# Optimization experiments

Hardware: AMD Instinct MI355X
Metric: run time of the kernel (lower is better)

The kernel has to match this reference:

```python
import jax, jax.numpy as jnp
import numpy as np

B, D_IN, D_HID, D_OUT = 16384, 512, 512, 512
E, K = 8, 2
VQ_COEFF, LB_COEFF = 0.05, 0.01
LOG100 = float(np.log(100.0))
LOG2 = float(np.log(2.0))


def _normalize(v):
    # torch F.normalize(dim=1): x / max(||x||, 1e-12)
    n = jnp.linalg.norm(v, axis=-1, keepdims=True)
    return v / jnp.maximum(n, 1e-12)


def _cv_squared(v):
    # torch .var() is unbiased (ddof=1)
    return jnp.var(v, ddof=1) / (jnp.mean(v) ** 2 + 1e-10)


def _rbm_layer(x, rm, W, b, ca, temp):
    # x: [B, d_in], rm: [E, d_in], W: [E, d_out, d_in], b: [E, d_out]
    rm_n = jax.lax.stop_gradient(_normalize(rm))          # .detach() in source
    nx = _normalize(x)
    dists = nx @ rm_n.T                                    # [B, E]
    top_v, top_i = jax.lax.top_k(dists, K)                 # [B, K]
    tv = jax.nn.softmax(top_v, axis=-1)                    # softmax over top-k
    bsz = dists.shape[0]
    attn = jnp.zeros_like(dists).at[jnp.arange(bsz)[:, None], top_i].set(tv)
    # const_attention is frozen (requires_grad=False)
    inp_att = jnp.exp(jnp.minimum(jax.lax.stop_gradient(ca), LOG100))  # [E]
    # dense gather-compute-scatter: expert e output for every token, masked by attn
    eo = jnp.einsum('bi,eoi->beo', x, W) * inp_att[None, :, None] + b[None, :, :]
    out = jnp.einsum('be,beo->bo', jax.lax.stop_gradient(attn), eo)    # att.detach()
    out = out * jnp.exp(jnp.minimum(temp, LOG100))
    # aux losses (eval mode: no EMA memory update)
    vq = -(nx[:, None, :] * rm_n[top_i]).sum(-1)           # [B, K]
    vq_loss = (tv * vq).sum(-1).mean()
    lb = _cv_squared(attn.sum(0))
    aux = VQ_COEFF * vq_loss + LB_COEFF * lb               # sim_coeff = 0
    return out, aux


def setup_inputs() -> dict:
    key = jax.random.key(0)
    ks = jax.random.split(key, 8)
    x = jax.random.normal(ks[0], (B, D_IN), dtype=jnp.float32)
    rm0 = _normalize(jax.random.normal(ks[1], (E, D_IN), dtype=jnp.float32))
    W0 = jax.random.normal(ks[2], (E, D_HID, D_IN), dtype=jnp.float32) / np.sqrt(D_IN)
    b0 = jnp.zeros((E, D_HID), dtype=jnp.float32)
    rm1 = _normalize(jax.random.normal(ks[3], (E, D_HID), dtype=jnp.float32))
    W1 = jax.random.normal(ks[4], (E, D_OUT, D_HID), dtype=jnp.float32) / np.sqrt(D_HID)
    b1 = jnp.zeros((E, D_OUT), dtype=jnp.float32)
    temp0 = jnp.full((1,), LOG2, dtype=jnp.float32)
    temp1 = jnp.full((1,), LOG2, dtype=jnp.float32)
    ca0 = jnp.zeros((E,), dtype=jnp.float32)
    ca1 = jnp.zeros((E,), dtype=jnp.float32)
    return {"x": x, "rm0": rm0, "W0": W0, "b0": b0, "temp0": temp0, "ca0": ca0,
            "rm1": rm1, "W1": W1, "b1": b1, "temp1": temp1, "ca1": ca1}


def reference(x, rm0, W0, b0, temp0, ca0, rm1, W1, b1, temp1, ca1):
    h0, a0 = _rbm_layer(x, rm0, W0, b0, ca0, temp0)
    h_emb = h0                      # embedding tapped after layer 0 (pre-activation)
    h = jax.nn.relu(h0)             # norm_type=None -> no norm
    h1, a1 = _rbm_layer(h, rm1, W1, b1, ca1, temp1)
    return (h_emb, h1, a0 + a1)
```

## Files before the change

kernel.cpp:

```cpp
#include <hip/hip_runtime.h>
#include <cmath>
#include <cstdint>

#define NTOK   16384
#define NEXP   8
#define DM     512
#define LOG100 4.605170185988092f

typedef _Float16 half8  __attribute__((ext_vector_type(8)));
typedef float    floatx4 __attribute__((ext_vector_type(4)));

#define MFMA_F16(a, b, c) __builtin_amdgcn_mfma_f32_16x16x32_f16((a), (b), (c), 0, 0, 0)

__device__ __forceinline__ void gl_lds16(const void* g, void* l) {
    __builtin_amdgcn_global_load_lds(
        (const __attribute__((address_space(1))) void*)g,
        (__attribute__((address_space(3))) void*)l, 16, 0, 0);
}

__device__ __forceinline__ void atomAddF(float* p, float v) {
#if __has_builtin(__builtin_amdgcn_global_atomic_fadd_f32)
    __builtin_amdgcn_global_atomic_fadd_f32((__attribute__((address_space(1))) float*)p, v);
#else
    atomicAdd(p, v);
#endif
}


__global__ __launch_bounds__(256) void pack_w_kernel(
    const float* __restrict__ W0, const float* __restrict__ W1,
    half8* __restrict__ w0pk, half8* __restrict__ w1pk,
    const float* __restrict__ rm0, const float* __restrict__ rm1,
    const float* __restrict__ ca0, const float* __restrict__ ca1,
    const float* __restrict__ temp0, const float* __restrict__ temp1,
    float* __restrict__ ctrl, float* __restrict__ rmn)
{
    if (blockIdx.x == 3072) {
        int tid = threadIdx.x, lane = tid & 63, w = tid >> 6;
        if (tid < 32) ((int*)ctrl)[tid] = 0;
        if (tid >= 32 && tid < 48) ctrl[tid] = 0.f;
        if (tid == 48 || tid == 49) ctrl[tid] = 0.f;
        if (tid == 50) ctrl[50] = expf(fminf(temp0[0], LOG100));
        if (tid == 51) ctrl[51] = expf(fminf(temp1[0], LOG100));
        if (tid >= 52 && tid < 68) {
            int i = tid - 52;
            ctrl[tid] = expf(fminf(i < 8 ? ca0[i] : ca1[i - 8], LOG100));
        }
        for (int r = w; r < 16; r += 4) {
            const float* src = (r < 8) ? (rm0 + r * DM) : (rm1 + (r - 8) * DM);
            float v[8]; float ss = 0.f;
            #pragma unroll
            for (int j = 0; j < 8; ++j) { v[j] = src[lane + 64 * j]; ss += v[j] * v[j]; }
            #pragma unroll
            for (int off = 32; off > 0; off >>= 1) ss += __shfl_xor(ss, off);
            float inv = 1.f / fmaxf(sqrtf(ss), 1e-12f);
            float* dst = rmn + r * DM;
            #pragma unroll
            for (int j = 0; j < 8; ++j) dst[lane + 64 * j] = v[j] * inv;
        }
        return;
    }
    int i = blockIdx.x * 256 + threadIdx.x;
    if (i < 512 * 1024) {
        int l = i & 63, j = (i >> 6) & 15, kb = (i >> 10) & 15, nt = (i >> 14) & 3, e = i >> 16;
        int s = l >> 3, p = l & 7, c = p ^ s;
        int n = nt * 128 + j * 8 + s;
        int k = kb * 32 + (c & 3) * 8;
        const float* src = W0 + ((size_t)e * DM + n) * DM + k;
        half8 v;
        #pragma unroll
        for (int t = 0; t < 8; ++t) {
            float f = src[t];
            _Float16 h = (_Float16)f;
            v[t] = (c < 4) ? h : (_Float16)(f - (float)h);
        }
        w0pk[i] = v;
    } else {
        int m = i - 512 * 1024;
        int l = m & 63, j = (m >> 6) & 15, kb = (m >> 10) & 7, nt = (m >> 13) & 3, e = m >> 15;
        int s = l >> 3, p = l & 7, c = p ^ s;
        int n = nt * 128 + j * 8 + s;
        int k = kb * 64 + c * 8;
        const float* src = W1 + ((size_t)e * DM + n) * DM + k;
        half8 v;
        #pragma unroll
        for (int t = 0; t < 8; ++t) v[t] = (_Float16)src[t];
        w1pk[m] = v;
    }
}

__global__ __launch_bounds__(256) void route_kernel(
    const float* __restrict__ src,
    const float* __restrict__ rmn,
    int relu_in, int split,
    _Float16* __restrict__ dst,
    unsigned char* __restrict__ key,
    float2* __restrict__ wts,
    float2* __restrict__ bs,
    float* __restrict__ zrow)
{
    __shared__ float rmLds[NEXP * DM];
    int tid = threadIdx.x;
    for (int i = tid; i < NEXP * DM; i += 256) rmLds[i] = rmn[i];
    __syncthreads();
    int lane = tid & 63, w = tid >> 6;
    int token = blockIdx.x * 4 + w;

    {
        float4 z4 = {0.f, 0.f, 0.f, 0.f};
        float4* zp = (float4*)(zrow + (size_t)token * DM);
        zp[lane] = z4;
        zp[lane + 64] = z4;
    }

    const float* row = src + (size_t)token * DM;
    float x[8]; float ss = 0.f;
    #pragma unroll
    for (int j = 0; j < 8; ++j) {
        float v = row[lane + 64 * j];
        if (relu_in) v = fmaxf(v, 0.f);
        x[j] = v; ss += v * v;
    }
    if (split) {
        #pragma unroll
        for (int j = 0; j < 8; ++j) {
            int k = lane + 64 * j;
            size_t base = (size_t)token * 1024 + (size_t)((k >> 5) << 6) + (k & 31);
            _Float16 h = (_Float16)x[j];
            dst[base] = h;
            dst[base + 32] = (_Float16)(x[j] - (float)h);
        }
    } else {
        #pragma unroll
        for (int j = 0; j < 8; ++j)
            dst[(size_t)token * DM + lane + 64 * j] = (_Float16)x[j];
    }
    float d[8];
    #pragma unroll
    for (int e = 0; e < 8; ++e) {
        float a = 0.f;
        #pragma unroll
        for (int j = 0; j < 8; ++j) a += x[j] * rmLds[e * DM + lane + 64 * j];
        d[e] = a;
    }
    #pragma unroll
    for (int off = 32; off > 0; off >>= 1) {
        ss += __shfl_xor(ss, off);
        #pragma unroll
        for (int e = 0; e < 8; ++e) d[e] += __shfl_xor(d[e], off);
    }
    float inv = 1.f / fmaxf(sqrtf(ss), 1e-12f);
    float best = -1e30f, second = -1e30f; int be = 0, se = 0;
    #pragma unroll
    for (int e = 0; e < 8; ++e) {
        float de = d[e] * inv;
        if (de > best)        { second = best; se = be; best = de; be = e; }
        else if (de > second) { second = de; se = e; }
    }
    float z = expf(second - best);
    float w0 = 1.f / (1.f + z), w1 = z / (1.f + z);
    if (lane == 0) {
        key[token] = (unsigned char)be;
        key[NTOK + token] = (unsigned char)se;
        wts[token] = make_float2(w0, w1);
        bs[token] = make_float2(best, second);
    }
}

__global__ __launch_bounds__(256) void compact_kernel(
    const unsigned char* __restrict__ key,
    const float2* __restrict__ wts,
    const float2* __restrict__ bs,
    int* __restrict__ cnt,
    unsigned short* __restrict__ bkt,
    float* __restrict__ imp,
    float* __restrict__ vq_acc)
{
    int slot = blockIdx.x >> 3, e = blockIdx.x & 7;
    int chunk = blockIdx.y;
    const unsigned char* k = key + slot * NTOK;
    unsigned short* ob = bkt + (size_t)(slot * 8 + e) * NTOK;
    int tid = threadIdx.x, lane = tid & 63, w = tid >> 6;
    float wsum = 0.f, vqs = 0.f;
    for (int c = 0; c < 8; ++c) {
        int tok = chunk * 2048 + c * 256 + tid;
        bool m = (k[tok] == (unsigned char)e);
        unsigned long long mask = __ballot(m);
        int wcount = __popcll(mask);
        int wbase = 0;
        if (lane == 0 && wcount) wbase = atomicAdd(&cnt[slot * 8 + e], wcount);
        wbase = __shfl(wbase, 0);
        if (m) {
            int pre = __popcll(mask & ((1ull << lane) - 1ull));
            ob[wbase + pre] = (unsigned short)tok;
            float2 wp = wts[tok]; float2 b2 = bs[tok];
            float wv = slot ? wp.y : wp.x;
            wsum += wv;
            vqs  += wv * (slot ? b2.y : b2.x);
        }
    }
    #pragma unroll
    for (int off = 32; off > 0; off >>= 1) {
        wsum += __shfl_xor(wsum, off);
        vqs  += __shfl_xor(vqs, off);
    }
    __shared__ float rw[4], rv[4];
    if (lane == 0) { rw[w] = wsum; rv[w] = vqs; }
    __syncthreads();
    if (tid == 0) {
        atomicAdd(&imp[e], rw[0] + rw[1] + rw[2] + rw[3]);
        atomicAdd(vq_acc, -(rv[0] + rv[1] + rv[2] + rv[3]));
    }
}

template <bool SPLIT>
__global__ __launch_bounds__(256, 4) void gemm_kernel(
    const _Float16* __restrict__ A,
    const _Float16* __restrict__ Wpk,
    const float* __restrict__ bias,
    const float* __restrict__ iav,
    const float* __restrict__ tscp,
    const int* __restrict__ cnt16,
    const unsigned short* __restrict__ bkt,
    const float2* __restrict__ wts,
    float* __restrict__ outp)
{
    __shared__ __align__(16) _Float16 ldsB[2 * 8192];
    __shared__ int tokLds[128];

    int p = blockIdx.x;
    int xcd = p & 7, s = p >> 3;
    int t = xcd * 34 + (s >> 2), nt = s & 3;
    int b = -1, m0 = 0, M = 0, acc0 = 0;
    #pragma unroll
    for (int bb = 0; bb < 16; ++bb) {
        int Me = cnt16[bb];
        int ne = (Me + 127) >> 7;
        if (t >= acc0 && t < acc0 + ne) { b = bb; m0 = (t - acc0) << 7; M = Me; }
        acc0 += ne;
    }
    if (b < 0) return;
    int slot = b >> 3, e = b & 7;
    int n0 = nt << 7;
    int valid = min(128, M - m0);
    int tid = threadIdx.x, lane = tid & 63, w = tid >> 6;
    if (tid < 128) tokLds[tid] = bkt[(size_t)b * NTOK + m0 + min(tid, valid - 1)];
    __syncthreads();

    int wm = w >> 1, wn = w & 1;
    int r0 = wm * 64, c0 = wn * 64;
    int q = lane >> 4, l15 = lane & 15;

    constexpr int KIT = SPLIT ? 16 : 8;
    constexpr int AS  = SPLIT ? 1024 : 512;

    const _Float16* Ab[4];
    #pragma unroll
    for (int mi = 0; mi < 4; ++mi)
        Ab[mi] = A + (size_t)tokLds[r0 + mi * 16 + l15] * AS + q * 8;

    const _Float16* wtile = Wpk + (size_t)(e * 4 + nt) * KIT * 8192;

    floatx4 accu[4][4];
    #pragma unroll
    for (int mi = 0; mi < 4; ++mi)
        #pragma unroll
        for (int ni = 0; ni < 4; ++ni) accu[mi][ni] = (floatx4){0.f, 0.f, 0.f, 0.f};

    #pragma unroll
    for (int jj = 0; jj < 4; ++jj) {
        int j = w + jj * 4;
        gl_lds16(wtile + j * 512 + lane * 8, (void*)(ldsB + j * 512));
    }

    #pragma unroll
    for (int kb = 0; kb < KIT; ++kb) {
        half8 ah[4], al[4];
        #pragma unroll
        for (int mi = 0; mi < 4; ++mi) {
            ah[mi] = *(const half8*)(Ab[mi] + kb * 64);
            al[mi] = *(const half8*)(Ab[mi] + kb * 64 + 32);
        }
        if (kb + 1 < KIT) {
            _Float16* dB = ldsB + ((kb + 1) & 1) * 8192;
            const _Float16* wb = wtile + (size_t)(kb + 1) * 8192;
            #pragma unroll
            for (int jj = 0; jj < 4; ++jj) {
                int j = w + jj * 4;
                gl_lds16(wb + j * 512 + lane * 8, (void*)(dB + j * 512));
            }
        }
        if (kb + 1 < KIT) asm volatile("s_waitcnt vmcnt(12)" ::: "memory");
        else              asm volatile("s_waitcnt vmcnt(8)"  ::: "memory");
        __builtin_amdgcn_sched_barrier(0);
        __builtin_amdgcn_s_barrier();
        {
            const _Float16* bB = ldsB + (kb & 1) * 8192;
            #pragma unroll
            for (int ni = 0; ni < 4; ++ni) {
                int r = c0 + ni * 16 + l15;
                int ph = q ^ (r & 7), pl = (q + 4) ^ (r & 7);
                half8 bh = *(const half8*)(bB + r * 64 + ph * 8);
                half8 bl = *(const half8*)(bB + r * 64 + pl * 8);
                if constexpr (SPLIT) {
                    #pragma unroll
                    for (int mi = 0; mi < 4; ++mi) accu[mi][ni] = MFMA_F16(ah[mi], bh, accu[mi][ni]);
                    #pragma unroll
                    for (int mi = 0; mi < 4; ++mi) accu[mi][ni] = MFMA_F16(ah[mi], bl, accu[mi][ni]);
                    #pragma unroll
                    for (int mi = 0; mi < 4; ++mi) accu[mi][ni] = MFMA_F16(al[mi], bh, accu[mi][ni]);
                } else {
                    #pragma unroll
                    for (int mi = 0; mi < 4; ++mi) accu[mi][ni] = MFMA_F16(ah[mi], bh, accu[mi][ni]);
                    #pragma unroll
                    for (int mi = 0; mi < 4; ++mi) accu[mi][ni] = MFMA_F16(al[mi], bl, accu[mi][ni]);
                }
            }
        }
        if (kb + 1 < KIT) {
            __builtin_amdgcn_sched_barrier(0);
            __builtin_amdgcn_s_barrier();
        }
    }

    float tsc = *tscp, iae = iav[e];
    float bv[4];
    #pragma unroll
    for (int ni = 0; ni < 4; ++ni) bv[ni] = bias[e * DM + n0 + c0 + ni * 16 + l15];
    #pragma unroll
    for (int mi = 0; mi < 4; ++mi) {
        int liBase = r0 + mi * 16 + q * 4;
        #pragma unroll
        for (int reg = 0; reg < 4; ++reg) {
            int li = liBase + reg;
            if (li < valid) {
                int tok = tokLds[li];
                float2 wp = wts[tok];
                float wgt = slot ? wp.y : wp.x;
                float sg = tsc * wgt * iae, sb = tsc * wgt;
                float* orow = outp + (size_t)tok * DM + n0;
                #pragma unroll
                for (int ni = 0; ni < 4; ++ni) {
                    float v = accu[mi][ni][reg] * sg + bv[ni] * sb;
                    int c = c0 + ni * 16 + l15;
                    atomAddF(&orow[c], v);
                }
            }
        }
    }
}

__global__ void finalize_kernel(const float* __restrict__ ctrl, float* __restrict__ outp)
{
    if (threadIdx.x == 0) {
        float aux = 0.f;
        for (int l = 0; l < 2; ++l) {
            float vq = ctrl[48 + l] / (float)NTOK;
            float mean = 0.f;
            for (int e = 0; e < 8; ++e) mean += ctrl[32 + l * 8 + e];
            mean *= 0.125f;
            float s = 0.f;
            for (int e = 0; e < 8; ++e) {
                float d = ctrl[32 + l * 8 + e] - mean;
                s += d * d;
            }
            float var = s / 7.f;
            float lb = var / (mean * mean + 1e-10f);
            aux += 0.05f * vq + 0.01f * lb;
        }
        *outp = aux;
    }
}

extern "C" void kernel_launch(void* const* d_in, const int* in_sizes, int n_in,
                              void* d_out, int out_size, void* d_ws, size_t ws_size,
                              hipStream_t stream) {
    const float* x     = (const float*)d_in[0];
    const float* rm0   = (const float*)d_in[1];
    const float* W0    = (const float*)d_in[2];
    const float* b0    = (const float*)d_in[3];
    const float* temp0 = (const float*)d_in[4];
    const float* ca0   = (const float*)d_in[5];
    const float* rm1   = (const float*)d_in[6];
    const float* W1    = (const float*)d_in[7];
    const float* b1    = (const float*)d_in[8];
    const float* temp1 = (const float*)d_in[9];
    const float* ca1   = (const float*)d_in[10];
    float* out = (float*)d_out;

    char* ws = (char*)d_ws;
    float* ctrl = (float*)ws;
    int*   cnt  = (int*)ctrl;
    float* imp  = ctrl + 32;
    float* vq   = ctrl + 48;
    float* tsc  = ctrl + 50;
    float* ia   = ctrl + 52;
    float* rmn  = ctrl + 128;
    float2*        wts = (float2*)(ws + (size_t)64  * 1024);
    float2*        bs  = (float2*)(ws + (size_t)384 * 1024);
    unsigned char* key = (unsigned char*)(ws + (size_t)704 * 1024);

    char* big = ws + (1 << 20);
    half8*          w0pk8 = (half8*)(big);
    half8*          w1pk8 = (half8*)(big + (size_t)8  * 1024 * 1024);
    const _Float16* w0pk  = (const _Float16*)w0pk8;
    const _Float16* w1pk  = (const _Float16*)w1pk8;
    _Float16*       h16   = (_Float16*)(big + (size_t)12 * 1024 * 1024);
    unsigned short* bkt   = (unsigned short*)(big + (size_t)28 * 1024 * 1024);

    _Float16* xpk = (_Float16*)(out + (size_t)NTOK * DM);

    pack_w_kernel<<<3073, 256, 0, stream>>>(W0, W1, w0pk8, w1pk8,
        rm0, rm1, ca0, ca1, temp0, temp1, ctrl, rmn);

    route_kernel<<<4096, 256, 0, stream>>>(x, rmn, 0, 1, xpk, key, wts, bs, out);
    compact_kernel<<<dim3(16, 8), 256, 0, stream>>>(key, wts, bs, cnt, bkt, imp, vq);
    gemm_kernel<true><<<1088, 256, 0, stream>>>(xpk, w0pk, b0, ia, tsc,
        cnt, bkt, wts, out);

    route_kernel<<<4096, 256, 0, stream>>>(out, rmn + 4096, 1, 0, h16,
        key + 2 * NTOK, wts + NTOK, bs + NTOK, out + (size_t)NTOK * DM);
    compact_kernel<<<dim3(16, 8), 256, 0, stream>>>(key + 2 * NTOK, wts + NTOK, bs + NTOK,
        cnt + 16, bkt + 16 * NTOK, imp + 8, vq + 1);
    gemm_kernel<false><<<1088, 256, 0, stream>>>(h16, w1pk, b1, ia + 8, tsc + 1,
        cnt + 16, bkt + 16 * NTOK, wts + NTOK, out + (size_t)NTOK * DM);

    finalize_kernel<<<1, 64, 0, stream>>>(ctrl, out + (size_t)2 * NTOK * DM);
}
```

Measured before the change: 460.6 us.

## Switch grouped GEMM to single-wave 64x64 tiles with register-prefetched A

The grouped expert GEMM changes from 256-thread blocks computing 128x128 tiles to single-wavefront blocks computing 64x64 tiles. The grid grows to 528*8 blocks and the XCD-aware block remapping is removed. Because one wave owns its LDS buffers, the per-k-step barriers go away. A-fragments are now double-buffered in registers so the next k-step's gathered A loads overlap the MFMAs. Each block reuses less of B and A, so global and L2 traffic rises and there are more redundant loads, in exchange for better load balance across uneven expert buckets and no barrier stalls.

```diff
diff --git a/kernel.cpp b/kernel.cpp
--- a/kernel.cpp
+++ b/kernel.cpp
@@ -214,7 +214,7 @@
 }
 
 template <bool SPLIT>
-__global__ __launch_bounds__(256, 4) void gemm_kernel(
+__global__ __launch_bounds__(64) void gemm_kernel(
     const _Float16* __restrict__ A,
     const _Float16* __restrict__ Wpk,
     const float* __restrict__ bias,
@@ -225,31 +225,27 @@
     const float2* __restrict__ wts,
     float* __restrict__ outp)
 {
-    __shared__ __align__(16) _Float16 ldsB[2 * 8192];
-    __shared__ int tokLds[128];
-
-    int p = blockIdx.x;
-    int xcd = p & 7, s = p >> 3;
-    int t = xcd * 34 + (s >> 2), nt = s & 3;
+    __shared__ __align__(16) _Float16 ldsB[2 * 4096];
+    __shared__ int tokLds[64];
+
+    int bx = blockIdx.x;
+    int t = bx >> 3, nt64 = bx & 7;
     int b = -1, m0 = 0, M = 0, acc0 = 0;
     #pragma unroll
     for (int bb = 0; bb < 16; ++bb) {
         int Me = cnt16[bb];
-        int ne = (Me + 127) >> 7;
-        if (t >= acc0 && t < acc0 + ne) { b = bb; m0 = (t - acc0) << 7; M = Me; }
+        int ne = (Me + 63) >> 6;
+        if (t >= acc0 && t < acc0 + ne) { b = bb; m0 = (t - acc0) << 6; M = Me; }
         acc0 += ne;
     }
     if (b < 0) return;
     int slot = b >> 3, e = b & 7;
-    int n0 = nt << 7;
-    int valid = min(128, M - m0);
-    int tid = threadIdx.x, lane = tid & 63, w = tid >> 6;
-    if (tid < 128) tokLds[tid] = bkt[(size_t)b * NTOK + m0 + min(tid, valid - 1)];
-    __syncthreads();
-
-    int wm = w >> 1, wn = w & 1;
-    int r0 = wm * 64, c0 = wn * 64;
+    int n0 = nt64 << 6;
+    int valid = min(64, M - m0);
+    int lane = threadIdx.x;
     int q = lane >> 4, l15 = lane & 15;
+
+    tokLds[lane] = bkt[(size_t)b * NTOK + m0 + min(lane, valid - 1)];
 
     constexpr int KIT = SPLIT ? 16 : 8;
     constexpr int AS  = SPLIT ? 1024 : 512;
@@ -257,9 +253,10 @@
     const _Float16* Ab[4];
     #pragma unroll
     for (int mi = 0; mi < 4; ++mi)
-        Ab[mi] = A + (size_t)tokLds[r0 + mi * 16 + l15] * AS + q * 8;
-
-    const _Float16* wtile = Wpk + (size_t)(e * 4 + nt) * KIT * 8192;
+        Ab[mi] = A + (size_t)tokLds[mi * 16 + l15] * AS + q * 8;
+
+    const _Float16* wtile = Wpk + ((size_t)(e * 4 + (nt64 >> 1)) * KIT) * 8192
+                                + (size_t)(nt64 & 1) * 8 * 512;
 
     floatx4 accu[4][4];
     #pragma unroll
@@ -267,69 +264,68 @@
         #pragma unroll
         for (int ni = 0; ni < 4; ++ni) accu[mi][ni] = (floatx4){0.f, 0.f, 0.f, 0.f};
 
-    #pragma unroll
-    for (int jj = 0; jj < 4; ++jj) {
-        int j = w + jj * 4;
-        gl_lds16(wtile + j * 512 + lane * 8, (void*)(ldsB + j * 512));
-    }
+    half8 ahR[2][4], alR[2][4];
+
+    #pragma unroll
+    for (int mi = 0; mi < 4; ++mi) {
+        ahR[0][mi] = *(const half8*)(Ab[mi]);
+        alR[0][mi] = *(const half8*)(Ab[mi] + 32);
+    }
+    #pragma unroll
+    for (int jj = 0; jj < 8; ++jj)
+        gl_lds16(wtile + jj * 512 + lane * 8, (void*)(ldsB + jj * 512));
 
     #pragma unroll
     for (int kb = 0; kb < KIT; ++kb) {
-        half8 ah[4], al[4];
-        #pragma unroll
-        for (int mi = 0; mi < 4; ++mi) {
-            ah[mi] = *(const half8*)(Ab[mi] + kb * 64);
-            al[mi] = *(const half8*)(Ab[mi] + kb * 64 + 32);
-        }
+        int cu = kb & 1, nx = cu ^ 1;
         if (kb + 1 < KIT) {
-            _Float16* dB = ldsB + ((kb + 1) & 1) * 8192;
+            #pragma unroll
+            for (int mi = 0; mi < 4; ++mi) {
+                ahR[nx][mi] = *(const half8*)(Ab[mi] + (kb + 1) * 64);
+                alR[nx][mi] = *(const half8*)(Ab[mi] + (kb + 1) * 64 + 32);
+            }
             const _Float16* wb = wtile + (size_t)(kb + 1) * 8192;
-            #pragma unroll
-            for (int jj = 0; jj < 4; ++jj) {
-                int j = w + jj * 4;
-                gl_lds16(wb + j * 512 + lane * 8, (void*)(dB + j * 512));
-            }
-        }
-        if (kb + 1 < KIT) asm volatile("s_waitcnt vmcnt(12)" ::: "memory");
-        else              asm volatile("s_waitcnt vmcnt(8)"  ::: "memory");
+            _Float16* dB = ldsB + nx * 4096;
+            #pragma unroll
+            for (int jj = 0; jj < 8; ++jj)
+                gl_lds16(wb + jj * 512 + lane * 8, (void*)(dB + jj * 512));
+            asm volatile("s_waitcnt vmcnt(16)" ::: "memory");
+        } else {
+            asm volatile("s_waitcnt vmcnt(0)" ::: "memory");
+        }
         __builtin_amdgcn_sched_barrier(0);
-        __builtin_amdgcn_s_barrier();
         {
-            const _Float16* bB = ldsB + (kb & 1) * 8192;
+            const _Float16* bB = ldsB + cu * 4096;
             #pragma unroll
             for (int ni = 0; ni < 4; ++ni) {
-                int r = c0 + ni * 16 + l15;
+                int r = ni * 16 + l15;
                 int ph = q ^ (r & 7), pl = (q + 4) ^ (r & 7);
                 half8 bh = *(const half8*)(bB + r * 64 + ph * 8);
                 half8 bl = *(const half8*)(bB + r * 64 + pl * 8);
                 if constexpr (SPLIT) {
                     #pragma unroll
-                    for (int mi = 0; mi < 4; ++mi) accu[mi][ni] = MFMA_F16(ah[mi], bh, accu[mi][ni]);
+                    for (int mi = 0; mi < 4; ++mi) accu[mi][ni] = MFMA_F16(ahR[cu][mi], bh, accu[mi][ni]);
                     #pragma unroll
-                    for (int mi = 0; mi < 4; ++mi) accu[mi][ni] = MFMA_F16(ah[mi], bl, accu[mi][ni]);
+                    for (int mi = 0; mi < 4; ++mi) accu[mi][ni] = MFMA_F16(ahR[cu][mi], bl, accu[mi][ni]);
                     #pragma unroll
-                    for (int mi = 0; mi < 4; ++mi) accu[mi][ni] = MFMA_F16(al[mi], bh, accu[mi][ni]);
+                    for (int mi = 0; mi < 4; ++mi) accu[mi][ni] = MFMA_F16(alR[cu][mi], bh, accu[mi][ni]);
                 } else {
                     #pragma unroll
-                    for (int mi = 0; mi < 4; ++mi) accu[mi][ni] = MFMA_F16(ah[mi], bh, accu[mi][ni]);
+                    for (int mi = 0; mi < 4; ++mi) accu[mi][ni] = MFMA_F16(ahR[cu][mi], bh, accu[mi][ni]);
                     #pragma unroll
-                    for (int mi = 0; mi < 4; ++mi) accu[mi][ni] = MFMA_F16(al[mi], bl, accu[mi][ni]);
+                    for (int mi = 0; mi < 4; ++mi) accu[mi][ni] = MFMA_F16(alR[cu][mi], bl, accu[mi][ni]);
                 }
             }
         }
-        if (kb + 1 < KIT) {
-            __builtin_amdgcn_sched_barrier(0);
-            __builtin_amdgcn_s_barrier();
-        }
     }
 
     float tsc = *tscp, iae = iav[e];
     float bv[4];
     #pragma unroll
-    for (int ni = 0; ni < 4; ++ni) bv[ni] = bias[e * DM + n0 + c0 + ni * 16 + l15];
+    for (int ni = 0; ni < 4; ++ni) bv[ni] = bias[e * DM + n0 + ni * 16 + l15];
     #pragma unroll
     for (int mi = 0; mi < 4; ++mi) {
-        int liBase = r0 + mi * 16 + q * 4;
+        int liBase = mi * 16 + q * 4;
         #pragma unroll
         for (int reg = 0; reg < 4; ++reg) {
             int li = liBase + reg;
@@ -342,7 +338,7 @@
                 #pragma unroll
                 for (int ni = 0; ni < 4; ++ni) {
                     float v = accu[mi][ni][reg] * sg + bv[ni] * sb;
-                    int c = c0 + ni * 16 + l15;
+                    int c = ni * 16 + l15;
                     atomAddF(&orow[c], v);
                 }
             }
@@ -410,19 +406,21 @@
 
     _Float16* xpk = (_Float16*)(out + (size_t)NTOK * DM);
 
+    const int GEMM_GRID = 528 * 8;
+
     pack_w_kernel<<<3073, 256, 0, stream>>>(W0, W1, w0pk8, w1pk8,
         rm0, rm1, ca0, ca1, temp0, temp1, ctrl, rmn);
 
     route_kernel<<<4096, 256, 0, stream>>>(x, rmn, 0, 1, xpk, key, wts, bs, out);
     compact_kernel<<<dim3(16, 8), 256, 0, stream>>>(key, wts, bs, cnt, bkt, imp, vq);
-    gemm_kernel<true><<<1088, 256, 0, stream>>>(xpk, w0pk, b0, ia, tsc,
+    gemm_kernel<true><<<GEMM_GRID, 64, 0, stream>>>(xpk, w0pk, b0, ia, tsc,
         cnt, bkt, wts, out);
 
     route_kernel<<<4096, 256, 0, stream>>>(out, rmn + 4096, 1, 0, h16,
         key + 2 * NTOK, wts + NTOK, bs + NTOK, out + (size_t)NTOK * DM);
     compact_kernel<<<dim3(16, 8), 256, 0, stream>>>(key + 2 * NTOK, wts + NTOK, bs + NTOK,
         cnt + 16, bkt + 16 * NTOK, imp + 8, vq + 1);
-    gemm_kernel<false><<<1088, 256, 0, stream>>>(h16, w1pk, b1, ia + 8, tsc + 1,
+    gemm_kernel<false><<<GEMM_GRID, 64, 0, stream>>>(h16, w1pk, b1, ia + 8, tsc + 1,
         cnt + 16, bkt + 16 * NTOK, wts + NTOK, out + (size_t)NTOK * DM);
 
     finalize_kernel<<<1, 64, 0, stream>>>(ctrl, out + (size_t)2 * NTOK * DM);
```

Result: faster. 450.5 us (-2.2%).
